# Kernel tuning notes

Hardware: AMD Instinct MI355X
Metric: run time of the kernel (lower is better)

Reference implementation:

```python
import jax, jax.numpy as jnp
import numpy as np

VISUAL_DIM = 4096
TEXT_DIM = 4096
EMBED_DIM = 2048
NUM_HEADS = 16
HEAD_DIM = EMBED_DIM // NUM_HEADS


def setup_inputs() -> dict:
    key = jax.random.key(0)
    ks = jax.random.split(key, 14)
    s = 0.02
    return {
        "visual_vec": jax.random.normal(ks[0], (VISUAL_DIM,), jnp.float32),
        "text_vec": jax.random.normal(ks[1], (TEXT_DIM,), jnp.float32),
        "q_w": jax.random.normal(ks[2], (EMBED_DIM, VISUAL_DIM), jnp.float32) * s,
        "q_b": jax.random.normal(ks[3], (EMBED_DIM,), jnp.float32) * s,
        "k_w": jax.random.normal(ks[4], (EMBED_DIM, TEXT_DIM), jnp.float32) * s,
        "k_b": jax.random.normal(ks[5], (EMBED_DIM,), jnp.float32) * s,
        "v_w": jax.random.normal(ks[6], (EMBED_DIM, TEXT_DIM), jnp.float32) * s,
        "v_b": jax.random.normal(ks[7], (EMBED_DIM,), jnp.float32) * s,
        "in_w": jax.random.normal(ks[8], (3 * EMBED_DIM, EMBED_DIM), jnp.float32) * s,
        "in_b": jax.random.normal(ks[9], (3 * EMBED_DIM,), jnp.float32) * s,
        "mo_w": jax.random.normal(ks[10], (EMBED_DIM, EMBED_DIM), jnp.float32) * s,
        "mo_b": jax.random.normal(ks[11], (EMBED_DIM,), jnp.float32) * s,
        "o_w": jax.random.normal(ks[12], (VISUAL_DIM, EMBED_DIM), jnp.float32) * s,
        "o_b": jax.random.normal(ks[13], (VISUAL_DIM,), jnp.float32) * s,
    }


def reference(visual_vec, text_vec, q_w, q_b, k_w, k_b, v_w, v_b,
              in_w, in_b, mo_w, mo_b, o_w, o_b):
    # Input projections (seq_len = batch = 1, so plain GEMVs)
    q = visual_vec @ q_w.T + q_b      # [E]
    k = text_vec @ k_w.T + k_b        # [E]
    v = text_vec @ v_w.T + v_b        # [E]

    # nn.MultiheadAttention in_proj (packed q/k/v weights)
    wq, wk, wv = jnp.split(in_w, 3, axis=0)
    bq, bk, bv = jnp.split(in_b, 3, axis=0)
    q2 = (q @ wq.T + bq).reshape(NUM_HEADS, 1, HEAD_DIM)  # [H,1,hd]
    k2 = (k @ wk.T + bk).reshape(NUM_HEADS, 1, HEAD_DIM)
    v2 = (v @ wv.T + bv).reshape(NUM_HEADS, 1, HEAD_DIM)

    scale = 1.0 / np.sqrt(HEAD_DIM).astype(np.float32)
    scores = jnp.einsum('hqd,hkd->hqk', q2, k2) * scale   # [H,1,1]
    attn = jax.nn.softmax(scores, axis=-1)                # trivially ones (kv_len=1)
    ctx = jnp.einsum('hqk,hkd->hqd', attn, v2).reshape(EMBED_DIM)

    attn_output = ctx @ mo_w.T + mo_b                     # MHA out_proj
    output = attn_output @ o_w.T + o_b                    # final out_proj
    return visual_vec + output
```

## Files before the change

### kernel.cpp

```cpp
#include <hip/hip_runtime.h>


#define ED 2048
#define VD 4096
#define NB 1024
#define NT 256

#define BAR_U 4224

__device__ __forceinline__ float wave_red(float v) {
#pragma unroll
    for (int off = 32; off > 0; off >>= 1) v += __shfl_down(v, off, 64);
    return v;
}

__device__ __forceinline__ void gload_lds16(const float* g, float* l) {
    __builtin_amdgcn_global_load_lds(
        (const __attribute__((address_space(1))) void*)g,
        (__attribute__((address_space(3))) void*)l, 16, 0, 0);
}

__device__ __forceinline__ void stage16k(const float* g, float* l, int wid, int lane) {
#pragma unroll
    for (int j = 0; j < 4; ++j) {
        const int c = wid * 4 + j;
        gload_lds16(g + c * 256 + lane * 4, l + c * 256);
    }
}

__device__ __forceinline__ void stage8k(const float* g, float* l, int wid, int lane) {
#pragma unroll
    for (int j = 0; j < 2; ++j) {
        const int c = wid * 2 + j;
        gload_lds16(g + c * 256 + lane * 4, l + c * 256);
    }
}

__device__ __forceinline__ void store_uc(float* p, float v) {
    union { float f; unsigned u; } c; c.f = v;
    __hip_atomic_store((unsigned*)p, c.u, __ATOMIC_RELAXED,
                       __HIP_MEMORY_SCOPE_SYSTEM);
}
__device__ __forceinline__ float2 load_uc2(const float* p) {
    union { unsigned long long u; float2 f; } c;
    c.u = __hip_atomic_load((const unsigned long long*)p, __ATOMIC_RELAXED,
                            __HIP_MEMORY_SCOPE_SYSTEM);
    return c.f;
}

__device__ __forceinline__ void barrier_arrive(unsigned* base, int b) {
    if (threadIdx.x == 0) {
        __asm__ volatile("s_waitcnt vmcnt(0)" ::: "memory");
        if (__hip_atomic_fetch_add(base + ((b >> 5) << 6), 1u,
                __ATOMIC_RELAXED, __HIP_MEMORY_SCOPE_SYSTEM) == 31u) {
            if (__hip_atomic_fetch_add(base + 2048, 1u,
                    __ATOMIC_RELAXED, __HIP_MEMORY_SCOPE_SYSTEM) == 31u) {
#pragma unroll
                for (int l = 0; l < 32; ++l)
                    __hip_atomic_store(base + 2112 + l * 64, 1u,
                                       __ATOMIC_RELAXED, __HIP_MEMORY_SCOPE_SYSTEM);
            }
        }
    }
}

__device__ __forceinline__ void barrier_wait(unsigned* base, int b) {
    if (threadIdx.x == 0) {
        unsigned* rel = base + 2112 + ((b >> 5) << 6);
        int spins = 0;
        while (__hip_atomic_load(rel, __ATOMIC_RELAXED,
                                 __HIP_MEMORY_SCOPE_SYSTEM) == 0u) {
            __builtin_amdgcn_s_sleep(4);
            if (++spins > (1 << 17)) break;
        }
    }
    __syncthreads();
}

__global__ __launch_bounds__(NT, 4)
void fused_chain(const float* __restrict__ visual,
                 const float* __restrict__ text,
                 const float* __restrict__ v_w,  const float* __restrict__ v_b,
                 const float* __restrict__ wv,   const float* __restrict__ bv,
                 const float* __restrict__ mo_w, const float* __restrict__ mo_b,
                 const float* __restrict__ o_w,  const float* __restrict__ o_b,
                 float* __restrict__ vvec, float* __restrict__ ctx,
                 float* __restrict__ attn, unsigned* __restrict__ flags,
                 float* __restrict__ out)
{
    __shared__ __align__(16) float sA[4096];
    __shared__ __align__(16) float sB[4096];
    __shared__ float red[16];

    const int t    = threadIdx.x;
    const int b    = blockIdx.x;
    const int lane = t & 63;
    const int wid  = t >> 6;
    const int r2   = 2 * b;
    const int r4   = 4 * b;

    const float4* A4 = (const float4*)sA;
    const float4* B4 = (const float4*)sB;

    stage16k(v_w + (size_t)r2 * VD,       sA, wid, lane);
    stage16k(v_w + (size_t)(r2 + 1) * VD, sB, wid, lane);
    const float4* x1p = (const float4*)text;
    float4 x1[4];
#pragma unroll
    for (int j = 0; j < 4; ++j) x1[j] = x1p[t + j * NT];
    __syncthreads();

    float a0 = 0.f, a1 = 0.f;
#pragma unroll
    for (int j = 0; j < 4; ++j) {
        float4 wa = A4[t + j * NT], wb = B4[t + j * NT];
        a0 = fmaf(wa.x, x1[j].x, a0); a0 = fmaf(wa.y, x1[j].y, a0);
        a0 = fmaf(wa.z, x1[j].z, a0); a0 = fmaf(wa.w, x1[j].w, a0);
        a1 = fmaf(wb.x, x1[j].x, a1); a1 = fmaf(wb.y, x1[j].y, a1);
        a1 = fmaf(wb.z, x1[j].z, a1); a1 = fmaf(wb.w, x1[j].w, a1);
    }
    float bi0 = 0.f, bi1 = 0.f;
    if (t == 0) { bi0 = v_b[r2]; bi1 = v_b[r2 + 1]; }
    a0 = wave_red(a0); a1 = wave_red(a1);
    if (lane == 0) { red[wid] = a0; red[8 + wid] = a1; }
    __syncthreads();
    if (t == 0) {
        store_uc(vvec + r2,     red[0] + red[1] + red[2] + red[3] + bi0);
        store_uc(vvec + r2 + 1, red[8] + red[9] + red[10] + red[11] + bi1);
    }
    barrier_arrive(flags, b);

    stage8k(wv + (size_t)r2 * ED,         sA,        wid, lane);
    stage8k(wv + (size_t)(r2 + 1) * ED,   sA + 2048, wid, lane);
    stage8k(mo_w + (size_t)r2 * ED,       sB,        wid, lane);
    stage8k(mo_w + (size_t)(r2 + 1) * ED, sB + 2048, wid, lane);

    barrier_wait(flags, b);

    float2 xl[2], xh[2];
#pragma unroll
    for (int j = 0; j < 2; ++j) {
        xl[j] = load_uc2(vvec + 4 * (t + j * NT));
        xh[j] = load_uc2(vvec + 4 * (t + j * NT) + 2);
    }
    a0 = 0.f; a1 = 0.f;
#pragma unroll
    for (int j = 0; j < 2; ++j) {
        float4 wa = A4[t + j * NT], wb = A4[512 + t + j * NT];
        a0 = fmaf(wa.x, xl[j].x, a0); a0 = fmaf(wa.y, xl[j].y, a0);
        a0 = fmaf(wa.z, xh[j].x, a0); a0 = fmaf(wa.w, xh[j].y, a0);
        a1 = fmaf(wb.x, xl[j].x, a1); a1 = fmaf(wb.y, xl[j].y, a1);
        a1 = fmaf(wb.z, xh[j].x, a1); a1 = fmaf(wb.w, xh[j].y, a1);
    }
    if (t == 0) { bi0 = bv[r2]; bi1 = bv[r2 + 1]; }
    a0 = wave_red(a0); a1 = wave_red(a1);
    if (lane == 0) { red[wid] = a0; red[8 + wid] = a1; }
    __syncthreads();
    if (t == 0) {
        store_uc(ctx + r2,     red[0] + red[1] + red[2] + red[3] + bi0);
        store_uc(ctx + r2 + 1, red[8] + red[9] + red[10] + red[11] + bi1);
    }
    barrier_arrive(flags + BAR_U, b);

    stage8k(o_w + (size_t)r4 * ED,       sA,        wid, lane);
    stage8k(o_w + (size_t)(r4 + 1) * ED, sA + 2048, wid, lane);

    barrier_wait(flags + BAR_U, b);

#pragma unroll
    for (int j = 0; j < 2; ++j) {
        xl[j] = load_uc2(ctx + 4 * (t + j * NT));
        xh[j] = load_uc2(ctx + 4 * (t + j * NT) + 2);
    }
    a0 = 0.f; a1 = 0.f;
#pragma unroll
    for (int j = 0; j < 2; ++j) {
        float4 wa = B4[t + j * NT], wb = B4[512 + t + j * NT];
        a0 = fmaf(wa.x, xl[j].x, a0); a0 = fmaf(wa.y, xl[j].y, a0);
        a0 = fmaf(wa.z, xh[j].x, a0); a0 = fmaf(wa.w, xh[j].y, a0);
        a1 = fmaf(wb.x, xl[j].x, a1); a1 = fmaf(wb.y, xl[j].y, a1);
        a1 = fmaf(wb.z, xh[j].x, a1); a1 = fmaf(wb.w, xh[j].y, a1);
    }
    if (t == 0) { bi0 = mo_b[r2]; bi1 = mo_b[r2 + 1]; }
    a0 = wave_red(a0); a1 = wave_red(a1);
    if (lane == 0) { red[wid] = a0; red[8 + wid] = a1; }
    __syncthreads();
    if (t == 0) {
        store_uc(attn + r2,     red[0] + red[1] + red[2] + red[3] + bi0);
        store_uc(attn + r2 + 1, red[8] + red[9] + red[10] + red[11] + bi1);
    }
    barrier_arrive(flags + 2 * BAR_U, b);

    stage8k(o_w + (size_t)(r4 + 2) * ED, sB,        wid, lane);
    stage8k(o_w + (size_t)(r4 + 3) * ED, sB + 2048, wid, lane);

    barrier_wait(flags + 2 * BAR_U, b);

#pragma unroll
    for (int j = 0; j < 2; ++j) {
        xl[j] = load_uc2(attn + 4 * (t + j * NT));
        xh[j] = load_uc2(attn + 4 * (t + j * NT) + 2);
    }
    float c0 = 0.f, c1 = 0.f, c2 = 0.f, c3 = 0.f;
#pragma unroll
    for (int j = 0; j < 2; ++j) {
        float4 wa = A4[t + j * NT], wb = A4[512 + t + j * NT];
        float4 wc = B4[t + j * NT], wd = B4[512 + t + j * NT];
        c0 = fmaf(wa.x, xl[j].x, c0); c0 = fmaf(wa.y, xl[j].y, c0);
        c0 = fmaf(wa.z, xh[j].x, c0); c0 = fmaf(wa.w, xh[j].y, c0);
        c1 = fmaf(wb.x, xl[j].x, c1); c1 = fmaf(wb.y, xl[j].y, c1);
        c1 = fmaf(wb.z, xh[j].x, c1); c1 = fmaf(wb.w, xh[j].y, c1);
        c2 = fmaf(wc.x, xl[j].x, c2); c2 = fmaf(wc.y, xl[j].y, c2);
        c2 = fmaf(wc.z, xh[j].x, c2); c2 = fmaf(wc.w, xh[j].y, c2);
        c3 = fmaf(wd.x, xl[j].x, c3); c3 = fmaf(wd.y, xl[j].y, c3);
        c3 = fmaf(wd.z, xh[j].x, c3); c3 = fmaf(wd.w, xh[j].y, c3);
    }
    float bo0 = 0.f, bo1 = 0.f, bo2 = 0.f, bo3 = 0.f;
    if (t == 0) {
        bo0 = o_b[r4] + visual[r4];
        bo1 = o_b[r4 + 1] + visual[r4 + 1];
        bo2 = o_b[r4 + 2] + visual[r4 + 2];
        bo3 = o_b[r4 + 3] + visual[r4 + 3];
    }
    c0 = wave_red(c0); c1 = wave_red(c1); c2 = wave_red(c2); c3 = wave_red(c3);
    if (lane == 0) {
        red[wid] = c0; red[4 + wid] = c1; red[8 + wid] = c2; red[12 + wid] = c3;
    }
    __syncthreads();
    if (t == 0) {
        out[r4]     = red[0]  + red[1]  + red[2]  + red[3]  + bo0;
        out[r4 + 1] = red[4]  + red[5]  + red[6]  + red[7]  + bo1;
        out[r4 + 2] = red[8]  + red[9]  + red[10] + red[11] + bo2;
        out[r4 + 3] = red[12] + red[13] + red[14] + red[15] + bo3;
    }
}

extern "C" void kernel_launch(void* const* d_in, const int* in_sizes, int n_in,
                              void* d_out, int out_size, void* d_ws, size_t ws_size,
                              hipStream_t stream) {
    (void)in_sizes; (void)n_in; (void)out_size; (void)ws_size;
    const float* visual = (const float*)d_in[0];
    const float* text   = (const float*)d_in[1];
    const float* v_w  = (const float*)d_in[6];
    const float* v_b  = (const float*)d_in[7];
    const float* in_w = (const float*)d_in[8];
    const float* in_b = (const float*)d_in[9];
    const float* mo_w = (const float*)d_in[10];
    const float* mo_b = (const float*)d_in[11];
    const float* o_w  = (const float*)d_in[12];
    const float* o_b  = (const float*)d_in[13];
    float* out = (float*)d_out;

    const float* wv = in_w + (size_t)2 * ED * ED;
    const float* bv = in_b + 2 * ED;

    float* ws   = (float*)d_ws;
    float* vvec = ws;
    float* ctx  = ws + ED;
    float* attn = ws + 2 * ED;
    unsigned* flags = (unsigned*)(ws + 8192);

    hipMemsetAsync(flags, 0, 3 * BAR_U * sizeof(unsigned), stream);
    fused_chain<<<NB, NT, 0, stream>>>(visual, text, v_w, v_b, wv, bv,
                                       mo_w, mo_b, o_w, o_b,
                                       vvec, ctx, attn, flags, out);
}
```

Before: 32.90 us.

## Specialize waves per stage and overlap weight staging with grid barriers

```diff
diff --git a/kernel.cpp b/kernel.cpp
--- a/kernel.cpp
+++ b/kernel.cpp
@@ -5,8 +5,10 @@
 #define VD 4096
 #define NB 1024
 #define NT 256
-
 #define BAR_U 4224
+
+#define SCHED_FENCE() __builtin_amdgcn_sched_barrier(0)
+#define BARRIER()     __builtin_amdgcn_s_barrier()
 
 __device__ __forceinline__ float wave_red(float v) {
 #pragma unroll
@@ -27,13 +29,10 @@
         gload_lds16(g + c * 256 + lane * 4, l + c * 256);
     }
 }
-
-__device__ __forceinline__ void stage8k(const float* g, float* l, int wid, int lane) {
-#pragma unroll
-    for (int j = 0; j < 2; ++j) {
-        const int c = wid * 2 + j;
+__device__ __forceinline__ void stage8k_1w(const float* g, float* l, int lane) {
+#pragma unroll
+    for (int c = 0; c < 8; ++c)
         gload_lds16(g + c * 256 + lane * 4, l + c * 256);
-    }
 }
 
 __device__ __forceinline__ void store_uc(float* p, float v) {
@@ -48,33 +47,27 @@
     return c.f;
 }
 
-__device__ __forceinline__ void barrier_arrive(unsigned* base, int b) {
-    if (threadIdx.x == 0) {
-        __asm__ volatile("s_waitcnt vmcnt(0)" ::: "memory");
-        if (__hip_atomic_fetch_add(base + ((b >> 5) << 6), 1u,
+__device__ __forceinline__ void arrive_tree(unsigned* base, int b) {
+    asm volatile("s_waitcnt vmcnt(0)" ::: "memory");
+    if (__hip_atomic_fetch_add(base + ((b >> 5) << 6), 1u,
+            __ATOMIC_RELAXED, __HIP_MEMORY_SCOPE_SYSTEM) == 31u) {
+        if (__hip_atomic_fetch_add(base + 2048, 1u,
                 __ATOMIC_RELAXED, __HIP_MEMORY_SCOPE_SYSTEM) == 31u) {
-            if (__hip_atomic_fetch_add(base + 2048, 1u,
-                    __ATOMIC_RELAXED, __HIP_MEMORY_SCOPE_SYSTEM) == 31u) {
-#pragma unroll
-                for (int l = 0; l < 32; ++l)
-                    __hip_atomic_store(base + 2112 + l * 64, 1u,
-                                       __ATOMIC_RELAXED, __HIP_MEMORY_SCOPE_SYSTEM);
-            }
-        }
-    }
-}
-
-__device__ __forceinline__ void barrier_wait(unsigned* base, int b) {
-    if (threadIdx.x == 0) {
-        unsigned* rel = base + 2112 + ((b >> 5) << 6);
-        int spins = 0;
-        while (__hip_atomic_load(rel, __ATOMIC_RELAXED,
-                                 __HIP_MEMORY_SCOPE_SYSTEM) == 0u) {
-            __builtin_amdgcn_s_sleep(4);
-            if (++spins > (1 << 17)) break;
-        }
-    }
-    __syncthreads();
+#pragma unroll
+            for (int l = 0; l < 32; ++l)
+                __hip_atomic_store(base + 2112 + l * 64, 1u,
+                                   __ATOMIC_RELAXED, __HIP_MEMORY_SCOPE_SYSTEM);
+        }
+    }
+}
+__device__ __forceinline__ void poll_release(unsigned* base, int b) {
+    unsigned* rel = base + 2112 + ((b >> 5) << 6);
+    int spins = 0;
+    while (__hip_atomic_load(rel, __ATOMIC_RELAXED,
+                             __HIP_MEMORY_SCOPE_SYSTEM) == 0u) {
+        __builtin_amdgcn_s_sleep(2);
+        if (++spins > (1 << 17)) break;
+    }
 }
 
 __global__ __launch_bounds__(NT, 4)
@@ -102,13 +95,29 @@
     const float4* A4 = (const float4*)sA;
     const float4* B4 = (const float4*)sB;
 
+    float bi10=0.f, bi11=0.f, bi20=0.f, bi21=0.f, bi30=0.f, bi31=0.f;
+    float bo0=0.f, bo1=0.f, bo2=0.f, bo3=0.f;
+    if (t == 0) {
+        bi10 = v_b[r2];  bi11 = v_b[r2+1];
+        bi20 = bv[r2];   bi21 = bv[r2+1];
+        bi30 = mo_b[r2]; bi31 = mo_b[r2+1];
+        bo0 = o_b[r4]   + visual[r4];
+        bo1 = o_b[r4+1] + visual[r4+1];
+        bo2 = o_b[r4+2] + visual[r4+2];
+        bo3 = o_b[r4+3] + visual[r4+3];
+    }
+
     stage16k(v_w + (size_t)r2 * VD,       sA, wid, lane);
     stage16k(v_w + (size_t)(r2 + 1) * VD, sB, wid, lane);
     const float4* x1p = (const float4*)text;
     float4 x1[4];
 #pragma unroll
     for (int j = 0; j < 4; ++j) x1[j] = x1p[t + j * NT];
-    __syncthreads();
+
+    asm volatile("s_waitcnt vmcnt(0)" ::: "memory");
+    SCHED_FENCE();
+    BARRIER();
+    SCHED_FENCE();
 
     float a0 = 0.f, a1 = 0.f;
 #pragma unroll
@@ -119,58 +128,76 @@
         a1 = fmaf(wb.x, x1[j].x, a1); a1 = fmaf(wb.y, x1[j].y, a1);
         a1 = fmaf(wb.z, x1[j].z, a1); a1 = fmaf(wb.w, x1[j].w, a1);
     }
-    float bi0 = 0.f, bi1 = 0.f;
-    if (t == 0) { bi0 = v_b[r2]; bi1 = v_b[r2 + 1]; }
     a0 = wave_red(a0); a1 = wave_red(a1);
     if (lane == 0) { red[wid] = a0; red[8 + wid] = a1; }
-    __syncthreads();
-    if (t == 0) {
-        store_uc(vvec + r2,     red[0] + red[1] + red[2] + red[3] + bi0);
-        store_uc(vvec + r2 + 1, red[8] + red[9] + red[10] + red[11] + bi1);
-    }
-    barrier_arrive(flags, b);
-
-    stage8k(wv + (size_t)r2 * ED,         sA,        wid, lane);
-    stage8k(wv + (size_t)(r2 + 1) * ED,   sA + 2048, wid, lane);
-    stage8k(mo_w + (size_t)r2 * ED,       sB,        wid, lane);
-    stage8k(mo_w + (size_t)(r2 + 1) * ED, sB + 2048, wid, lane);
-
-    barrier_wait(flags, b);
+    asm volatile("s_waitcnt lgkmcnt(0)" ::: "memory");
+    SCHED_FENCE();
+    BARRIER();
+    SCHED_FENCE();
+
+    if (wid == 1) {
+        stage8k_1w(wv + (size_t)r2 * ED,         sA,        lane);
+        stage8k_1w(wv + (size_t)(r2 + 1) * ED,   sA + 2048, lane);
+        stage8k_1w(mo_w + (size_t)r2 * ED,       sB,        lane);
+        stage8k_1w(mo_w + (size_t)(r2 + 1) * ED, sB + 2048, lane);
+    }
+    if (t == 0) {
+        store_uc(vvec + r2,     red[0] + red[1] + red[2] + red[3] + bi10);
+        store_uc(vvec + r2 + 1, red[8] + red[9] + red[10] + red[11] + bi11);
+        arrive_tree(flags, b);
+        poll_release(flags, b);
+    }
+
+    float2 x2a[8], x2b[8];
+    if (wid == 0) {
+#pragma unroll
+        for (int j = 0; j < 8; ++j) {
+            const float* p = vvec + 4 * (lane + j * 64);
+            x2a[j] = load_uc2(p); x2b[j] = load_uc2(p + 2);
+        }
+    }
+
+    if (wid == 1) { asm volatile("s_waitcnt vmcnt(16)" ::: "memory"); }
+    else          { asm volatile("s_waitcnt vmcnt(0)"  ::: "memory"); }
+    SCHED_FENCE();
+    BARRIER();
+    SCHED_FENCE();
+
+    if (wid == 0) {
+        float s20 = 0.f, s21 = 0.f;
+#pragma unroll
+        for (int j = 0; j < 8; ++j) {
+            float4 wa = A4[lane + j * 64];
+            float4 wb = A4[512 + lane + j * 64];
+            s20 = fmaf(wa.x, x2a[j].x, s20); s20 = fmaf(wa.y, x2a[j].y, s20);
+            s20 = fmaf(wa.z, x2b[j].x, s20); s20 = fmaf(wa.w, x2b[j].y, s20);
+            s21 = fmaf(wb.x, x2a[j].x, s21); s21 = fmaf(wb.y, x2a[j].y, s21);
+            s21 = fmaf(wb.z, x2b[j].x, s21); s21 = fmaf(wb.w, x2b[j].y, s21);
+        }
+        s20 = wave_red(s20); s21 = wave_red(s21);
+        if (t == 0) {
+            store_uc(ctx + r2,     s20 + bi20);
+            store_uc(ctx + r2 + 1, s21 + bi21);
+            arrive_tree(flags + BAR_U, b);
+            poll_release(flags + BAR_U, b);
+        }
+    }
+
+    asm volatile("s_waitcnt vmcnt(0)" ::: "memory");
+    SCHED_FENCE();
+    BARRIER();
+    SCHED_FENCE();
 
     float2 xl[2], xh[2];
 #pragma unroll
     for (int j = 0; j < 2; ++j) {
-        xl[j] = load_uc2(vvec + 4 * (t + j * NT));
-        xh[j] = load_uc2(vvec + 4 * (t + j * NT) + 2);
-    }
-    a0 = 0.f; a1 = 0.f;
-#pragma unroll
-    for (int j = 0; j < 2; ++j) {
-        float4 wa = A4[t + j * NT], wb = A4[512 + t + j * NT];
-        a0 = fmaf(wa.x, xl[j].x, a0); a0 = fmaf(wa.y, xl[j].y, a0);
-        a0 = fmaf(wa.z, xh[j].x, a0); a0 = fmaf(wa.w, xh[j].y, a0);
-        a1 = fmaf(wb.x, xl[j].x, a1); a1 = fmaf(wb.y, xl[j].y, a1);
-        a1 = fmaf(wb.z, xh[j].x, a1); a1 = fmaf(wb.w, xh[j].y, a1);
-    }
-    if (t == 0) { bi0 = bv[r2]; bi1 = bv[r2 + 1]; }
-    a0 = wave_red(a0); a1 = wave_red(a1);
-    if (lane == 0) { red[wid] = a0; red[8 + wid] = a1; }
-    __syncthreads();
-    if (t == 0) {
-        store_uc(ctx + r2,     red[0] + red[1] + red[2] + red[3] + bi0);
-        store_uc(ctx + r2 + 1, red[8] + red[9] + red[10] + red[11] + bi1);
-    }
-    barrier_arrive(flags + BAR_U, b);
-
-    stage8k(o_w + (size_t)r4 * ED,       sA,        wid, lane);
-    stage8k(o_w + (size_t)(r4 + 1) * ED, sA + 2048, wid, lane);
-
-    barrier_wait(flags + BAR_U, b);
-
-#pragma unroll
-    for (int j = 0; j < 2; ++j) {
-        xl[j] = load_uc2(ctx + 4 * (t + j * NT));
-        xh[j] = load_uc2(ctx + 4 * (t + j * NT) + 2);
+        const float* p = ctx + 4 * (t + j * NT);
+        xl[j] = load_uc2(p); xh[j] = load_uc2(p + 2);
+    }
+    SCHED_FENCE();
+    if (wid == 2) {
+        stage8k_1w(o_w + (size_t)r4 * ED,       sA,        lane);
+        stage8k_1w(o_w + (size_t)(r4 + 1) * ED, sA + 2048, lane);
     }
     a0 = 0.f; a1 = 0.f;
 #pragma unroll
@@ -181,25 +208,33 @@
         a1 = fmaf(wb.x, xl[j].x, a1); a1 = fmaf(wb.y, xl[j].y, a1);
         a1 = fmaf(wb.z, xh[j].x, a1); a1 = fmaf(wb.w, xh[j].y, a1);
     }
-    if (t == 0) { bi0 = mo_b[r2]; bi1 = mo_b[r2 + 1]; }
     a0 = wave_red(a0); a1 = wave_red(a1);
     if (lane == 0) { red[wid] = a0; red[8 + wid] = a1; }
-    __syncthreads();
-    if (t == 0) {
-        store_uc(attn + r2,     red[0] + red[1] + red[2] + red[3] + bi0);
-        store_uc(attn + r2 + 1, red[8] + red[9] + red[10] + red[11] + bi1);
-    }
-    barrier_arrive(flags + 2 * BAR_U, b);
-
-    stage8k(o_w + (size_t)(r4 + 2) * ED, sB,        wid, lane);
-    stage8k(o_w + (size_t)(r4 + 3) * ED, sB + 2048, wid, lane);
-
-    barrier_wait(flags + 2 * BAR_U, b);
-
-#pragma unroll
-    for (int j = 0; j < 2; ++j) {
-        xl[j] = load_uc2(attn + 4 * (t + j * NT));
-        xh[j] = load_uc2(attn + 4 * (t + j * NT) + 2);
+    asm volatile("s_waitcnt lgkmcnt(0)" ::: "memory");
+    SCHED_FENCE();
+    BARRIER();
+    SCHED_FENCE();
+
+    if (t == 0) {
+        store_uc(attn + r2,     red[0] + red[1] + red[2] + red[3] + bi30);
+        store_uc(attn + r2 + 1, red[8] + red[9] + red[10] + red[11] + bi31);
+        arrive_tree(flags + 2 * BAR_U, b);
+    }
+    if (wid == 3) {
+        stage8k_1w(o_w + (size_t)(r4 + 2) * ED, sB,        lane);
+        stage8k_1w(o_w + (size_t)(r4 + 3) * ED, sB + 2048, lane);
+    }
+    if (t == 0) poll_release(flags + 2 * BAR_U, b);
+
+    asm volatile("s_waitcnt vmcnt(0)" ::: "memory");
+    SCHED_FENCE();
+    BARRIER();
+    SCHED_FENCE();
+
+#pragma unroll
+    for (int j = 0; j < 2; ++j) {
+        const float* p = attn + 4 * (t + j * NT);
+        xl[j] = load_uc2(p); xh[j] = load_uc2(p + 2);
     }
     float c0 = 0.f, c1 = 0.f, c2 = 0.f, c3 = 0.f;
 #pragma unroll
@@ -215,18 +250,14 @@
         c3 = fmaf(wd.x, xl[j].x, c3); c3 = fmaf(wd.y, xl[j].y, c3);
         c3 = fmaf(wd.z, xh[j].x, c3); c3 = fmaf(wd.w, xh[j].y, c3);
     }
-    float bo0 = 0.f, bo1 = 0.f, bo2 = 0.f, bo3 = 0.f;
-    if (t == 0) {
-        bo0 = o_b[r4] + visual[r4];
-        bo1 = o_b[r4 + 1] + visual[r4 + 1];
-        bo2 = o_b[r4 + 2] + visual[r4 + 2];
-        bo3 = o_b[r4 + 3] + visual[r4 + 3];
-    }
     c0 = wave_red(c0); c1 = wave_red(c1); c2 = wave_red(c2); c3 = wave_red(c3);
     if (lane == 0) {
         red[wid] = c0; red[4 + wid] = c1; red[8 + wid] = c2; red[12 + wid] = c3;
     }
-    __syncthreads();
+    asm volatile("s_waitcnt lgkmcnt(0)" ::: "memory");
+    SCHED_FENCE();
+    BARRIER();
+    SCHED_FENCE();
     if (t == 0) {
         out[r4]     = red[0]  + red[1]  + red[2]  + red[3]  + bo0;
         out[r4 + 1] = red[4]  + red[5]  + red[6]  + red[7]  + bo1;
```

Measured after the change: 34.21 us. 4.0% more time.
